# Optimization experiments

Measured on AMD Instinct MI355X. Metric: run time of the kernel, lower is better.

The kernel has to match this reference:

```python
import jax, jax.numpy as jnp
import numpy as np

B, SEQ_LEN, CHANNELS, PRED_LEN = 64, 1024, 512, 720
KERNEL = 25
PAD = (KERNEL - 1) // 2  # 12
IN_LEN = SEQ_LEN // 2    # 512
INV_SQRT2 = 1.0 / np.sqrt(2.0).astype(np.float32)


def dct2_ortho_matrix(N):
    # Orthonormal DCT-II basis: X_k = s_k * sum_n x_n cos(pi*(n+0.5)*k/N)
    n = np.arange(N, dtype=np.float64)
    k = np.arange(N, dtype=np.float64)
    M = np.cos(np.pi * (n[None, :] + 0.5) * k[:, None] / N)
    scale = np.sqrt(2.0 / N) * np.ones(N)
    scale[0] = np.sqrt(1.0 / N)
    return jnp.asarray((scale[:, None] * M).astype(np.float32))  # [k, n]


def setup_inputs() -> dict:
    key = jax.random.key(0)
    k1, k2, k3, k4, k5 = jax.random.split(key, 5)
    bound = 1.0 / np.sqrt(IN_LEN)
    return {
        "x": jax.random.normal(k1, (B, SEQ_LEN, CHANNELS), dtype=jnp.float32),
        "W_seasonal": jax.random.uniform(k2, (PRED_LEN, IN_LEN), jnp.float32, -bound, bound),
        "b_seasonal": jax.random.uniform(k3, (PRED_LEN,), jnp.float32, -bound, bound),
        "W_trend": jax.random.uniform(k4, (PRED_LEN, IN_LEN), jnp.float32, -bound, bound),
        "b_trend": jax.random.uniform(k5, (PRED_LEN,), jnp.float32, -bound, bound),
    }


def reference(x, W_seasonal, b_seasonal, W_trend, b_trend):
    # --- series decomposition: moving average (edge-padded, window 25) ---
    padded = jnp.pad(x, ((0, 0), (PAD, PAD), (0, 0)), mode="edge")  # [B, L+24, C]
    cs = jnp.cumsum(padded, axis=1)
    cs = jnp.pad(cs, ((0, 0), (1, 0), (0, 0)))  # leading zero, [B, L+25, C]
    trend = (cs[:, KERNEL:, :] - cs[:, :-KERNEL, :]) / KERNEL  # [B, L, C]
    seasonal = x - trend

    # [B, C, L]
    s = jnp.transpose(seasonal, (0, 2, 1))
    t = jnp.transpose(trend, (0, 2, 1))

    # --- grouped conv1d with [1,1]/sqrt(2), stride 2 (Haar low-pass downsample) ---
    def down(v):
        return (v[..., 0::2] + v[..., 1::2]) * INV_SQRT2  # [B, C, L/2]

    s = down(s)
    t = down(t)

    # --- orthonormal DCT-II over last axis, then divide by length ---
    Mdct = dct2_ortho_matrix(IN_LEN)  # [k, n]
    s = jnp.einsum("bcn,kn->bck", s, Mdct) / IN_LEN
    t = jnp.einsum("bcn,kn->bck", t, Mdct) / IN_LEN

    # --- shared Linear per branch ---
    s_out = jnp.einsum("bck,pk->bcp", s, W_seasonal) + b_seasonal
    t_out = jnp.einsum("bck,pk->bcp", t, W_trend) + b_trend

    out = s_out + t_out  # [B, C, pred_len]
    return jnp.transpose(out, (0, 2, 1))  # [B, pred_len, C]
```

## Files before the change

### kernel.cpp

```cpp
#include <hip/hip_runtime.h>
#include <hip/hip_bf16.h>
#include <math.h>


#define BATCH 64
#define SEQ 1024
#define CH 512
#define PRED 720
#define INV_SQRT2 0.70710678118654752440f

typedef __attribute__((ext_vector_type(4))) float floatx4;
typedef __attribute__((ext_vector_type(8))) short bf16x8;

#define KBF_OFF   0ull
#define BIAS_OFF  1572864ull
#define MW_OFF    1575936ull
#define WEFFS_OFF 2624512ull
#define WEFFT_OFF 4099072ull
#define XT_OFF    5573632ull
#define WS_NEED   (XT_OFF + 67108864ull)

__global__ void build_M(float* __restrict__ Mw) {
    int idx = blockIdx.x * 256 + threadIdx.x;
    int k = idx >> 9, n = idx & 511;
    int m = ((2 * n + 1) * k) & 2047;
    float ang = (float)m * (float)(M_PI / 1024.0);
    float scale = (k == 0) ? 0.04419417382415922f
                           : 0.0625f;
    Mw[idx] = cosf(ang) * scale * (1.0f / 512.0f);
}

__global__ void __launch_bounds__(256) build_weff(
    const float* __restrict__ Ws_in, const float* __restrict__ Wt_in,
    const float* __restrict__ Mw,
    float* __restrict__ outS, float* __restrict__ outT) {
    const float* W = blockIdx.z ? Wt_in : Ws_in;
    float* out     = blockIdx.z ? outT  : outS;
    int n0 = blockIdx.x * 64;
    int p0 = blockIdx.y * 64;
    int t  = threadIdx.x;
    int tx = t & 15, ty = t >> 4;
    __shared__ float wlds[32][65];
    __shared__ float mlds[32][64];
    float a[4][4] = {};
    for (int kb = 0; kb < 512; kb += 32) {
        __syncthreads();
        {
            int pp = t >> 2, kk0 = (t & 3) * 8;
            int prow = min(p0 + pp, PRED - 1);
            const float* wsrc = &W[(size_t)prow * 512 + kb + kk0];
#pragma unroll
            for (int e = 0; e < 8; e++) wlds[kk0 + e][pp] = wsrc[e];
        }
        {
            int kk = t >> 3, nn = (t & 7) * 8;
            const float* msrc = &Mw[(size_t)(kb + kk) * 512 + n0 + nn];
            *reinterpret_cast<floatx4*>(&mlds[kk][nn])     = *reinterpret_cast<const floatx4*>(&msrc[0]);
            *reinterpret_cast<floatx4*>(&mlds[kk][nn + 4]) = *reinterpret_cast<const floatx4*>(&msrc[4]);
        }
        __syncthreads();
#pragma unroll
        for (int kk = 0; kk < 32; kk++) {
            floatx4 wv = *reinterpret_cast<const floatx4*>(&wlds[kk][ty * 4]);
            floatx4 mv = *reinterpret_cast<const floatx4*>(&mlds[kk][tx * 4]);
#pragma unroll
            for (int i = 0; i < 4; i++)
#pragma unroll
                for (int j = 0; j < 4; j++)
                    a[i][j] += wv[i] * mv[j];
        }
    }
#pragma unroll
    for (int i = 0; i < 4; i++) {
        int p = p0 + ty * 4 + i;
        if (p < PRED) {
            floatx4 v = {a[i][0], a[i][1], a[i][2], a[i][3]};
            *reinterpret_cast<floatx4*>(&out[(size_t)p * 512 + n0 + tx * 4]) = v;
        }
    }
}

__device__ __forceinline__ int tcnt(int j, int l) {
    if (l == 0)    return max(0, 13 - j);
    if (l == 1023) return max(0, j - 1010);
    int d = l - j; if (d < 0) d = -d;
    return (d <= 12) ? 1 : 0;
}

__global__ void build_kmat(const float* __restrict__ Ws, const float* __restrict__ Wt,
                           const float* __restrict__ bs, const float* __restrict__ bt,
                           __hip_bfloat16* __restrict__ Kbf, float* __restrict__ bias) {
    int idx = blockIdx.x * 256 + threadIdx.x;
    int p = idx >> 10, l = idx & 1023;
    if (p >= PRED) { Kbf[idx] = __float2bfloat16(0.0f); return; }
    if (l == 0) bias[p] = bs[p] + bt[p];
    float v = INV_SQRT2 * Ws[(size_t)p * 512 + (l >> 1)];
    int jlo = max(0, l - 12), jhi = min(1023, l + 12);
    float acc = 0.f;
    for (int n = (jlo >> 1); n <= (jhi >> 1); n++) {
        int c = tcnt(2 * n, l) + tcnt(2 * n + 1, l);
        if (c) acc += (Wt[(size_t)p * 512 + n] - Ws[(size_t)p * 512 + n]) * (float)c;
    }
    v += acc * (INV_SQRT2 / 25.0f);
    Kbf[idx] = __float2bfloat16(v);
}

__device__ __forceinline__ void async_ld16(const void* g, void* l) {
    __builtin_amdgcn_global_load_lds((const __attribute__((address_space(1))) void*)g,
                                     (__attribute__((address_space(3))) void*)l, 16, 0, 0);
}

__device__ __forceinline__ short f2bf(float f) {
    __hip_bfloat16 h = __float2bfloat16(f);
    return *reinterpret_cast<short*>(&h);
}

__global__ void __launch_bounds__(256) xpose(const float* __restrict__ x,
                                             short* __restrict__ xT) {
    __shared__ float lds[64][65];
    int t = threadIdx.x;
    int l0 = blockIdx.x * 64, c0 = blockIdx.y * 64, b = blockIdx.z;
    const float* xb = x + (size_t)b * SEQ * CH;
    int row4 = t >> 4, cq = t & 15;
#pragma unroll
    for (int i = 0; i < 4; i++) {
        int row = row4 + i * 16;
        floatx4 v = __builtin_nontemporal_load(reinterpret_cast<const floatx4*>(
            xb + (size_t)(l0 + row) * CH + c0 + cq * 4));
#pragma unroll
        for (int e = 0; e < 4; e++) lds[row][cq * 4 + e] = v[e];
    }
    __syncthreads();
    size_t outb = (size_t)b * CH * SEQ;
#pragma unroll
    for (int r = 0; r < 2; r++) {
        int u = r * 256 + t;
        int lr = u & 7, c = u >> 3;
        bf16x8 s;
#pragma unroll
        for (int e = 0; e < 8; e++) s[e] = f2bf(lds[lr * 8 + e][c]);
        *reinterpret_cast<bf16x8*>(&xT[outb + (size_t)(c0 + c) * SEQ + l0 + lr * 8]) = s;
    }
}

__global__ void __launch_bounds__(256, 3) gemm_main_t(
    const short* __restrict__ Kbf, const short* __restrict__ xT,
    const float* __restrict__ bias, float* __restrict__ out) {
    __shared__ __align__(16) short ldsbuf[3 * 2 * 128 * 32];
    int t = threadIdx.x;
    int wave = t >> 6, lane = t & 63;
    int bid = blockIdx.x;
    int work = (bid & 7) * 192 + (bid >> 3);
    int mt = work % 6;
    int grp = work / 6;
    int nt = grp & 3, b = grp >> 2;
    int wm = wave >> 1, wn = wave & 1;
    const short* Ag = Kbf + (size_t)mt * 128 * 1024;
    const short* Bg = xT + ((size_t)b * CH + nt * 128) * 1024;

    size_t srcoff[2];
#pragma unroll
    for (int rdi = 0; rdi < 2; rdi++) {
        int q = rdi * 256 + t;
        int row = ((q >> 6) << 4) + (q & 15);
        int ko = ((q >> 4) & 3) * 8;
        srcoff[rdi] = (size_t)row * 1024 + ko;
    }

    floatx4 acc[4][4];
#pragma unroll
    for (int i = 0; i < 4; i++)
#pragma unroll
        for (int j = 0; j < 4; j++)
            acc[i][j] = (floatx4){0.f, 0.f, 0.f, 0.f};

#pragma unroll
    for (int s = 0; s < 2; s++) {
        char* base = (char*)ldsbuf + s * 16384;
        int k0 = s * 32;
#pragma unroll
        for (int rdi = 0; rdi < 2; rdi++) {
            char* dA = base + rdi * 4096 + wave * 1024;
            async_ld16(Ag + srcoff[rdi] + k0, dA);
            async_ld16(Bg + srcoff[rdi] + k0, dA + 8192);
        }
    }

    int cur = 0, nx2 = 2;
    for (int it = 0; it < 31; ++it) {
        asm volatile("s_waitcnt vmcnt(4)" ::: "memory");
        __builtin_amdgcn_s_barrier();
        __builtin_amdgcn_sched_barrier(0);
        if (it < 30) {
            int k0n = (it + 2) * 32;
            char* base = (char*)ldsbuf + nx2 * 16384;
#pragma unroll
            for (int rdi = 0; rdi < 2; rdi++) {
                char* dA = base + rdi * 4096 + wave * 1024;
                async_ld16(Ag + srcoff[rdi] + k0n, dA);
                async_ld16(Bg + srcoff[rdi] + k0n, dA + 8192);
            }
        }
        const char* cb = (const char*)ldsbuf + cur * 16384;
        bf16x8 af[4], bf[4];
#pragma unroll
        for (int i = 0; i < 4; i++)
            af[i] = *reinterpret_cast<const bf16x8*>(cb + ((wm * 4 + i) << 10) + (lane << 4));
#pragma unroll
        for (int j = 0; j < 4; j++)
            bf[j] = *reinterpret_cast<const bf16x8*>(cb + 8192 + ((wn * 4 + j) << 10) + (lane << 4));
        __builtin_amdgcn_s_setprio(1);
#pragma unroll
        for (int i = 0; i < 4; i++)
#pragma unroll
            for (int j = 0; j < 4; j++)
                acc[i][j] = __builtin_amdgcn_mfma_f32_16x16x32_bf16(af[i], bf[j], acc[i][j], 0, 0, 0);
        __builtin_amdgcn_s_setprio(0);
        cur = (cur == 2) ? 0 : cur + 1;
        nx2 = (nx2 == 2) ? 0 : nx2 + 1;
    }
    asm volatile("s_waitcnt vmcnt(0)" ::: "memory");
    __builtin_amdgcn_s_barrier();
    __builtin_amdgcn_sched_barrier(0);
    {
        const char* cb = (const char*)ldsbuf + cur * 16384;
        bf16x8 af[4], bf[4];
#pragma unroll
        for (int i = 0; i < 4; i++)
            af[i] = *reinterpret_cast<const bf16x8*>(cb + ((wm * 4 + i) << 10) + (lane << 4));
#pragma unroll
        for (int j = 0; j < 4; j++)
            bf[j] = *reinterpret_cast<const bf16x8*>(cb + 8192 + ((wn * 4 + j) << 10) + (lane << 4));
#pragma unroll
        for (int i = 0; i < 4; i++)
#pragma unroll
            for (int j = 0; j < 4; j++)
                acc[i][j] = __builtin_amdgcn_mfma_f32_16x16x32_bf16(af[i], bf[j], acc[i][j], 0, 0, 0);
    }

    int lm = lane & 15, kq = lane >> 4;
    int p0r = mt * 128 + wm * 64;
    int cb2 = nt * 128 + wn * 64 + lm;
    size_t outb = (size_t)b * PRED * CH;
#pragma unroll
    for (int i = 0; i < 4; i++) {
#pragma unroll
        for (int r = 0; r < 4; r++) {
            int p = p0r + i * 16 + kq * 4 + r;
            if (p < PRED) {
                float bv = bias[p];
#pragma unroll
                for (int j = 0; j < 4; j++)
                    __builtin_nontemporal_store(acc[i][j][r] + bv,
                                                &out[outb + (size_t)p * CH + cb2 + j * 16]);
            }
        }
    }
}

__global__ void __launch_bounds__(256) gemm_main(
    const short* __restrict__ Kbf, const float* __restrict__ x,
    const float* __restrict__ bias, float* __restrict__ out) {
    __shared__ __align__(16) short ldsA[128 * 32];
    int t = threadIdx.x;
    int wave = t >> 6, lane = t & 63;
    int mt = blockIdx.x % 6, nt = blockIdx.x / 6;
    int b  = blockIdx.y;
    int wm = wave >> 1, wn = wave & 1;
    const short* Ag = Kbf + (size_t)mt * 128 * 1024;
    const float* xb = x + (size_t)b * SEQ * CH;
    int lm = lane & 15, kq = lane >> 4;
    int cj[4];
    for (int j = 0; j < 4; j++) cj[j] = nt * 128 + wn * 64 + j * 16 + lm;

    floatx4 acc[4][4];
    for (int i = 0; i < 4; i++)
        for (int j = 0; j < 4; j++)
            acc[i][j] = (floatx4){0.f, 0.f, 0.f, 0.f};

    for (int k0 = 0; k0 < 1024; k0 += 32) {
        for (int rdi = 0; rdi < 2; rdi++) {
            int q = rdi * 256 + t;
            int row = q >> 2, ko = (q & 3) * 8;
            async_ld16(Ag + (size_t)row * 1024 + k0 + ko,
                       (char*)ldsA + rdi * 4096 + wave * 1024);
        }
        bf16x8 bfrag[4];
        int krow = k0 + kq * 8;
#pragma unroll
        for (int j = 0; j < 4; j++) {
            const float* xc = xb + (size_t)krow * CH + cj[j];
            bf16x8 bv;
#pragma unroll
            for (int i = 0; i < 8; i++) bv[i] = f2bf(xc[(size_t)i * CH]);
            bfrag[j] = bv;
        }
        __syncthreads();
        bf16x8 af[4];
        for (int i = 0; i < 4; i++)
            af[i] = *(const bf16x8*)&ldsA[(wm * 64 + i * 16 + lm) * 32 + kq * 8];
        for (int i = 0; i < 4; i++)
            for (int j = 0; j < 4; j++)
                acc[i][j] = __builtin_amdgcn_mfma_f32_16x16x32_bf16(af[i], bfrag[j], acc[i][j], 0, 0, 0);
        __syncthreads();
    }

    int p0 = mt * 128 + wm * 64;
    size_t outb = (size_t)b * PRED * CH;
    for (int i = 0; i < 4; i++) {
        for (int r = 0; r < 4; r++) {
            int p = p0 + i * 16 + kq * 4 + r;
            if (p < PRED) {
                float bv = bias[p];
                for (int j = 0; j < 4; j++) {
                    out[outb + (size_t)p * CH + cj[j]] = acc[i][j][r] + bv;
                }
            }
        }
    }
}

extern "C" void kernel_launch(void* const* d_in, const int* in_sizes, int n_in,
                              void* d_out, int out_size, void* d_ws, size_t ws_size,
                              hipStream_t stream) {
    const float* xp = nullptr; const float* wp[2] = {nullptr, nullptr};
    const float* bp[2] = {nullptr, nullptr};
    int wn = 0, bn = 0;
    for (int i = 0; i < n_in; i++) {
        if (in_sizes[i] == 33554432) xp = (const float*)d_in[i];
        else if (in_sizes[i] == 368640 && wn < 2) wp[wn++] = (const float*)d_in[i];
        else if (in_sizes[i] == 720 && bn < 2) bp[bn++] = (const float*)d_in[i];
    }
    if (!xp || wn != 2 || bn != 2) {
        xp = (const float*)d_in[0]; wp[0] = (const float*)d_in[1];
        bp[0] = (const float*)d_in[2]; wp[1] = (const float*)d_in[3];
        bp[1] = (const float*)d_in[4];
    }
    float* out = (float*)d_out;

    char* ws = (char*)d_ws;
    __hip_bfloat16* Kbf = (__hip_bfloat16*)(ws + KBF_OFF);
    float* bias  = (float*)(ws + BIAS_OFF);
    float* Mw    = (float*)(ws + MW_OFF);
    float* WeffS = (float*)(ws + WEFFS_OFF);
    float* WeffT = (float*)(ws + WEFFT_OFF);
    short* xT    = (short*)(ws + XT_OFF);

    bool big = (ws_size >= (size_t)WS_NEED);

    if (big) xpose<<<dim3(16, 8, 64), 256, 0, stream>>>(xp, xT);
    build_M<<<1024, 256, 0, stream>>>(Mw);
    build_weff<<<dim3(8, 12, 2), 256, 0, stream>>>(wp[0], wp[1], Mw, WeffS, WeffT);
    build_kmat<<<3072, 256, 0, stream>>>(WeffS, WeffT, bp[0], bp[1], Kbf, bias);
    if (big)
        gemm_main_t<<<1536, 256, 0, stream>>>((const short*)Kbf, (const short*)xT, bias, out);
    else
        gemm_main<<<dim3(24, 64), 256, 0, stream>>>((const short*)Kbf, xp, bias, out);
}
```

Baseline: 368.0 us.

## Enlarge GEMM tile to 128x256 with 8 waves, BK=64, and fuse DCT matrix build

The main GEMM moves from 256-thread 128x128 tiles with 32-wide K steps to 512-thread 128x256 tiles with 64-wide K steps. This halves the block count and the number of barrier iterations, and reuses each A tile across twice as many columns. The separate build_M kernel is removed and the DCT cosines are computed inline inside build_weff, saving one launch and a global round trip. The cost is more LDS per block (three 48KB stages), which limits occupancy to about two blocks per CU and leaves fewer blocks for load balance.

```diff
diff --git a/kernel.cpp b/kernel.cpp
--- a/kernel.cpp
+++ b/kernel.cpp
@@ -20,19 +20,8 @@
 #define XT_OFF    5573632ull
 #define WS_NEED   (XT_OFF + 67108864ull)
 
-__global__ void build_M(float* __restrict__ Mw) {
-    int idx = blockIdx.x * 256 + threadIdx.x;
-    int k = idx >> 9, n = idx & 511;
-    int m = ((2 * n + 1) * k) & 2047;
-    float ang = (float)m * (float)(M_PI / 1024.0);
-    float scale = (k == 0) ? 0.04419417382415922f
-                           : 0.0625f;
-    Mw[idx] = cosf(ang) * scale * (1.0f / 512.0f);
-}
-
 __global__ void __launch_bounds__(256) build_weff(
     const float* __restrict__ Ws_in, const float* __restrict__ Wt_in,
-    const float* __restrict__ Mw,
     float* __restrict__ outS, float* __restrict__ outT) {
     const float* W = blockIdx.z ? Wt_in : Ws_in;
     float* out     = blockIdx.z ? outT  : outS;
@@ -53,10 +42,18 @@
             for (int e = 0; e < 8; e++) wlds[kk0 + e][pp] = wsrc[e];
         }
         {
-            int kk = t >> 3, nn = (t & 7) * 8;
-            const float* msrc = &Mw[(size_t)(kb + kk) * 512 + n0 + nn];
-            *reinterpret_cast<floatx4*>(&mlds[kk][nn])     = *reinterpret_cast<const floatx4*>(&msrc[0]);
-            *reinterpret_cast<floatx4*>(&mlds[kk][nn + 4]) = *reinterpret_cast<const floatx4*>(&msrc[4]);
+            int kk = t >> 3, nn0 = (t & 7) * 8;
+            int k = kb + kk;
+            float scale = (k == 0) ? 0.04419417382415922f
+                                   : 0.0625f;
+            scale *= (1.0f / 512.0f);
+#pragma unroll
+            for (int e = 0; e < 8; e++) {
+                int n = n0 + nn0 + e;
+                int m = ((2 * n + 1) * k) & 2047;
+                float ang = (float)m * (float)(M_PI / 1024.0);
+                mlds[kk][nn0 + e] = cosf(ang) * scale;
+            }
         }
         __syncthreads();
 #pragma unroll
@@ -143,28 +140,26 @@
     }
 }
 
-__global__ void __launch_bounds__(256, 3) gemm_main_t(
+__global__ void __launch_bounds__(512, 2) gemm_main_t(
     const short* __restrict__ Kbf, const short* __restrict__ xT,
     const float* __restrict__ bias, float* __restrict__ out) {
-    __shared__ __align__(16) short ldsbuf[3 * 2 * 128 * 32];
+    __shared__ __align__(16) short ldsbuf[3 * 24576];
     int t = threadIdx.x;
     int wave = t >> 6, lane = t & 63;
     int bid = blockIdx.x;
-    int work = (bid & 7) * 192 + (bid >> 3);
+    int work = (bid & 7) * 96 + (bid >> 3);
     int mt = work % 6;
-    int grp = work / 6;
-    int nt = grp & 3, b = grp >> 2;
-    int wm = wave >> 1, wn = wave & 1;
+    int nt = work / 6;
+    int wm = wave >> 2, wn = wave & 3;
     const short* Ag = Kbf + (size_t)mt * 128 * 1024;
-    const short* Bg = xT + ((size_t)b * CH + nt * 128) * 1024;
-
-    size_t srcoff[2];
-#pragma unroll
-    for (int rdi = 0; rdi < 2; rdi++) {
-        int q = rdi * 256 + t;
-        int row = ((q >> 6) << 4) + (q & 15);
-        int ko = ((q >> 4) & 3) * 8;
-        srcoff[rdi] = (size_t)row * 1024 + ko;
+    const short* Bg = xT + (size_t)nt * 256 * 1024;
+
+    size_t so[4];
+#pragma unroll
+    for (int a = 0; a < 4; a++) {
+        int s = a * 512 + t;
+        so[a] = (size_t)(((s >> 7) << 4) + (s & 15)) * 1024
+              + ((s >> 6) & 1) * 32 + ((s >> 4) & 3) * 8;
     }
 
     floatx4 acc[4][4];
@@ -174,48 +169,48 @@
         for (int j = 0; j < 4; j++)
             acc[i][j] = (floatx4){0.f, 0.f, 0.f, 0.f};
 
-#pragma unroll
-    for (int s = 0; s < 2; s++) {
-        char* base = (char*)ldsbuf + s * 16384;
-        int k0 = s * 32;
-#pragma unroll
-        for (int rdi = 0; rdi < 2; rdi++) {
-            char* dA = base + rdi * 4096 + wave * 1024;
-            async_ld16(Ag + srcoff[rdi] + k0, dA);
-            async_ld16(Bg + srcoff[rdi] + k0, dA + 8192);
-        }
-    }
+#define STAGE(bufidx, k0v)                                                     \
+    {                                                                          \
+        char* base_ = (char*)ldsbuf + (bufidx) * 49152;                        \
+        _Pragma("unroll")                                                      \
+        for (int a = 0; a < 2; a++)                                            \
+            async_ld16(Ag + so[a] + (k0v),                                     \
+                       base_ + (a * 512 + wave * 64) * 16);                    \
+        _Pragma("unroll")                                                      \
+        for (int a = 0; a < 4; a++)                                            \
+            async_ld16(Bg + so[a] + (k0v),                                     \
+                       base_ + 16384 + (a * 512 + wave * 64) * 16);            \
+    }
+
+    STAGE(0, 0);
+    STAGE(1, 64);
 
     int cur = 0, nx2 = 2;
-    for (int it = 0; it < 31; ++it) {
-        asm volatile("s_waitcnt vmcnt(4)" ::: "memory");
+    for (int it = 0; it < 15; ++it) {
+        asm volatile("s_waitcnt vmcnt(6)" ::: "memory");
         __builtin_amdgcn_s_barrier();
         __builtin_amdgcn_sched_barrier(0);
-        if (it < 30) {
-            int k0n = (it + 2) * 32;
-            char* base = (char*)ldsbuf + nx2 * 16384;
-#pragma unroll
-            for (int rdi = 0; rdi < 2; rdi++) {
-                char* dA = base + rdi * 4096 + wave * 1024;
-                async_ld16(Ag + srcoff[rdi] + k0n, dA);
-                async_ld16(Bg + srcoff[rdi] + k0n, dA + 8192);
-            }
-        }
-        const char* cb = (const char*)ldsbuf + cur * 16384;
-        bf16x8 af[4], bf[4];
-#pragma unroll
-        for (int i = 0; i < 4; i++)
-            af[i] = *reinterpret_cast<const bf16x8*>(cb + ((wm * 4 + i) << 10) + (lane << 4));
-#pragma unroll
-        for (int j = 0; j < 4; j++)
-            bf[j] = *reinterpret_cast<const bf16x8*>(cb + 8192 + ((wn * 4 + j) << 10) + (lane << 4));
-        __builtin_amdgcn_s_setprio(1);
-#pragma unroll
-        for (int i = 0; i < 4; i++)
+        if (it < 14) STAGE(nx2, (it + 2) * 64);
+        const char* cb = (const char*)ldsbuf + cur * 49152;
+#pragma unroll
+        for (int ks = 0; ks < 2; ks++) {
+            bf16x8 af[4], bf[4];
+#pragma unroll
+            for (int i = 0; i < 4; i++)
+                af[i] = *reinterpret_cast<const bf16x8*>(
+                    cb + ((wm * 4 + i) << 11) + (ks << 10) + (lane << 4));
 #pragma unroll
             for (int j = 0; j < 4; j++)
-                acc[i][j] = __builtin_amdgcn_mfma_f32_16x16x32_bf16(af[i], bf[j], acc[i][j], 0, 0, 0);
-        __builtin_amdgcn_s_setprio(0);
+                bf[j] = *reinterpret_cast<const bf16x8*>(
+                    cb + 16384 + ((wn * 4 + j) << 11) + (ks << 10) + (lane << 4));
+            __builtin_amdgcn_s_setprio(1);
+#pragma unroll
+            for (int i = 0; i < 4; i++)
+#pragma unroll
+                for (int j = 0; j < 4; j++)
+                    acc[i][j] = __builtin_amdgcn_mfma_f32_16x16x32_bf16(af[i], bf[j], acc[i][j], 0, 0, 0);
+            __builtin_amdgcn_s_setprio(0);
+        }
         cur = (cur == 2) ? 0 : cur + 1;
         nx2 = (nx2 == 2) ? 0 : nx2 + 1;
     }
@@ -223,24 +218,31 @@
     __builtin_amdgcn_s_barrier();
     __builtin_amdgcn_sched_barrier(0);
     {
-        const char* cb = (const char*)ldsbuf + cur * 16384;
-        bf16x8 af[4], bf[4];
-#pragma unroll
-        for (int i = 0; i < 4; i++)
-            af[i] = *reinterpret_cast<const bf16x8*>(cb + ((wm * 4 + i) << 10) + (lane << 4));
-#pragma unroll
-        for (int j = 0; j < 4; j++)
-            bf[j] = *reinterpret_cast<const bf16x8*>(cb + 8192 + ((wn * 4 + j) << 10) + (lane << 4));
-#pragma unroll
-        for (int i = 0; i < 4; i++)
+        const char* cb = (const char*)ldsbuf + cur * 49152;
+#pragma unroll
+        for (int ks = 0; ks < 2; ks++) {
+            bf16x8 af[4], bf[4];
+#pragma unroll
+            for (int i = 0; i < 4; i++)
+                af[i] = *reinterpret_cast<const bf16x8*>(
+                    cb + ((wm * 4 + i) << 11) + (ks << 10) + (lane << 4));
 #pragma unroll
             for (int j = 0; j < 4; j++)
-                acc[i][j] = __builtin_amdgcn_mfma_f32_16x16x32_bf16(af[i], bf[j], acc[i][j], 0, 0, 0);
-    }
+                bf[j] = *reinterpret_cast<const bf16x8*>(
+                    cb + 16384 + ((wn * 4 + j) << 11) + (ks << 10) + (lane << 4));
+#pragma unroll
+            for (int i = 0; i < 4; i++)
+#pragma unroll
+                for (int j = 0; j < 4; j++)
+                    acc[i][j] = __builtin_amdgcn_mfma_f32_16x16x32_bf16(af[i], bf[j], acc[i][j], 0, 0, 0);
+        }
+    }
+#undef STAGE
 
     int lm = lane & 15, kq = lane >> 4;
     int p0r = mt * 128 + wm * 64;
-    int cb2 = nt * 128 + wn * 64 + lm;
+    int b   = nt >> 1;
+    int cb2 = (nt & 1) * 256 + wn * 64 + lm;
     size_t outb = (size_t)b * PRED * CH;
 #pragma unroll
     for (int i = 0; i < 4; i++) {
@@ -341,7 +343,6 @@
     char* ws = (char*)d_ws;
     __hip_bfloat16* Kbf = (__hip_bfloat16*)(ws + KBF_OFF);
     float* bias  = (float*)(ws + BIAS_OFF);
-    float* Mw    = (float*)(ws + MW_OFF);
     float* WeffS = (float*)(ws + WEFFS_OFF);
     float* WeffT = (float*)(ws + WEFFT_OFF);
     short* xT    = (short*)(ws + XT_OFF);
@@ -349,11 +350,10 @@
     bool big = (ws_size >= (size_t)WS_NEED);
 
     if (big) xpose<<<dim3(16, 8, 64), 256, 0, stream>>>(xp, xT);
-    build_M<<<1024, 256, 0, stream>>>(Mw);
-    build_weff<<<dim3(8, 12, 2), 256, 0, stream>>>(wp[0], wp[1], Mw, WeffS, WeffT);
+    build_weff<<<dim3(8, 12, 2), 256, 0, stream>>>(wp[0], wp[1], WeffS, WeffT);
     build_kmat<<<3072, 256, 0, stream>>>(WeffS, WeffT, bp[0], bp[1], Kbf, bias);
     if (big)
-        gemm_main_t<<<1536, 256, 0, stream>>>((const short*)Kbf, (const short*)xT, bias, out);
+        gemm_main_t<<<768, 512, 0, stream>>>((const short*)Kbf, (const short*)xT, bias, out);
     else
         gemm_main<<<dim3(24, 64), 256, 0, stream>>>((const short*)Kbf, xp, bias, out);
 }
```

After: 349.7 us. 1.05x faster.
